# Performance work log

Measured on AMD Instinct MI355X. Metric: run time of the kernel, lower is better.

Reference implementation:

```python
import jax, jax.numpy as jnp
import numpy as np

B = 8
D_IN = 1024
DIM = 256
H = 8
HD = DIM // H
SIZES = [32768, 8192, 2048]
NUM_LEVELS = 3


def setup_inputs() -> dict:
    key = jax.random.key(0)
    ks = jax.random.split(key, 12)
    def p(k, shape, scale=0.02):
        return jax.random.normal(k, shape, dtype=jnp.float32) * scale
    return {
        "x": jax.random.normal(ks[0], (B, D_IN), dtype=jnp.float32),
        "proj_w": p(ks[1], (NUM_LEVELS, DIM, D_IN)),
        "proj_b": p(ks[2], (NUM_LEVELS, DIM)),
        "mem0": p(ks[3], (SIZES[0], DIM), 0.05),
        "mem1": p(ks[4], (SIZES[1], DIM), 0.05),
        "mem2": p(ks[5], (SIZES[2], DIM), 0.05),
        "inw": p(ks[6], (NUM_LEVELS, 3 * DIM, DIM)),
        "inb": p(ks[7], (NUM_LEVELS, 3 * DIM)),
        "outw": p(ks[8], (NUM_LEVELS, DIM, DIM)),
        "outb": p(ks[9], (NUM_LEVELS, DIM)),
        "merg_w": p(ks[10], (D_IN, NUM_LEVELS * DIM)),
        "merg_b": p(ks[11], (D_IN,)),
    }


def _forward(x, proj_w, proj_b, mems, inw, inb, outw, outb, merg_w, merg_b):
    level_outputs = []
    updated_memories = []
    scale = 1.0 / np.sqrt(HD).astype(np.float32)
    for i in range(NUM_LEVELS):
        # per-level projection of x: [B, DIM]
        p = x @ proj_w[i].T + proj_b[i]
        mem = mems[i]  # [S, DIM] (shared across batch, prev_memories=None path)
        wq, wk, wv = inw[i][:DIM], inw[i][DIM:2 * DIM], inw[i][2 * DIM:]
        bq, bk, bv = inb[i][:DIM], inb[i][DIM:2 * DIM], inb[i][2 * DIM:]
        q = (p @ wq.T + bq).reshape(B, H, HD)            # [B, H, HD]
        k = (mem @ wk.T + bk).reshape(-1, H, HD)         # [S, H, HD]
        v = (mem @ wv.T + bv).reshape(-1, H, HD)         # [S, H, HD]
        # single-query attention over the memory bank
        scores = jnp.einsum("bhd,shd->bhs", q, k) * scale   # [B, H, S]
        attn = jax.nn.softmax(scores, axis=-1)
        o = jnp.einsum("bhs,shd->bhd", attn, v).reshape(B, DIM)
        o = o @ outw[i].T + outb[i]                      # attention out_proj
        level_outputs.append(o)
        # broadcast memory update: [B, S, DIM]
        updated_memories.append(mem[None, :, :] + p[:, None, :])
    combined = jnp.concatenate(level_outputs, axis=-1)  # [B, 3*DIM]
    out = combined @ merg_w.T + merg_b                   # [B, D_IN]
    return (out, updated_memories[0], updated_memories[1], updated_memories[2])


def reference(x, proj_w, proj_b, mem0, mem1, mem2, inw, inb, outw, outb, merg_w, merg_b):
    return _forward(x, proj_w, proj_b, (mem0, mem1, mem2), inw, inb, outw, outb, merg_w, merg_b)
```

## Files before the change

### kernel.cpp

```cpp
#include <hip/hip_runtime.h>
#include <math.h>

#define BATCH 8
#define SCALE 0.17677669529663687f

#define WS_P    0
#define WS_QT   6144
#define WS_QBK  55296
#define WS_NUM  55488
#define WS_DEN  104640
#define WS_LVL  104832
#define WS_END  110976
#define WS_ZN   (WS_DEN + 192 - WS_NUM)

#define UM0_F4 2048u
#define UM1_F4 16779264u
#define UM2_F4 20973568u

typedef float f4 __attribute__((ext_vector_type(4)));

__global__ __launch_bounds__(1024) void kA(const float* __restrict__ x,
                                           const float* __restrict__ proj_w,
                                           const float* __restrict__ proj_b,
                                           const float* __restrict__ inw,
                                           const float* __restrict__ inb,
                                           float* __restrict__ ws) {
    const int i = blockIdx.x, b = blockIdx.y, t = threadIdx.x;
    __shared__ __align__(16) float xs[1024];
    __shared__ __align__(16) float ps[256];
    __shared__ __align__(16) float qs[256];
    const int o = t >> 2, part = t & 3;

    {
        const int bid = i * 8 + b;
        const int base = bid * 2056;
        #pragma unroll
        for (int rep = 0; rep < 3; ++rep) {
            const int k = base + rep * 1024 + t;
            if (k < base + 2056 && k < WS_ZN) ws[WS_NUM + k] = 0.f;
        }
    }

    xs[t] = x[b * 1024 + t];
    __syncthreads();

    {
        const f4* w4 = reinterpret_cast<const f4*>(proj_w + (size_t)i * 262144 + (size_t)o * 1024) + part * 64;
        const f4* x4 = reinterpret_cast<const f4*>(xs) + part * 64;
        float acc = 0.f;
        #pragma unroll 8
        for (int c = 0; c < 64; ++c) {
            f4 w = w4[c], xv = x4[c];
            acc += w.x * xv.x + w.y * xv.y + w.z * xv.z + w.w * xv.w;
        }
        acc += __shfl_xor(acc, 1);
        acc += __shfl_xor(acc, 2);
        if (part == 0) {
            const float p = acc + proj_b[i * 256 + o];
            ps[o] = p;
            ws[WS_P + i * 2048 + b * 256 + o] = p;
        }
    }
    __syncthreads();

    {
        const f4* w4 = reinterpret_cast<const f4*>(inw + (size_t)i * 196608 + (size_t)o * 256) + part * 16;
        const f4* p4 = reinterpret_cast<const f4*>(ps) + part * 16;
        float acc = 0.f;
        #pragma unroll
        for (int c = 0; c < 16; ++c) {
            f4 w = w4[c], pv = p4[c];
            acc += w.x * pv.x + w.y * pv.y + w.z * pv.z + w.w * pv.w;
        }
        acc += __shfl_xor(acc, 1);
        acc += __shfl_xor(acc, 2);
        if (part == 0) qs[o] = acc + inb[i * 768 + o];
    }
    __syncthreads();

    #pragma unroll
    for (int rep = 0; rep < 2; ++rep) {
        const int idx = rep * 1024 + t;
        const int h = idx >> 8, c = idx & 255;
        const float* wk = inw + (size_t)i * 196608 + (size_t)(256 + h * 32) * 256 + c;
        float acc = 0.f;
        #pragma unroll
        for (int d = 0; d < 32; ++d) acc += qs[h * 32 + d] * wk[(size_t)d * 256];
        ws[WS_QT + i * 16384 + (b * 8 + h) * 256 + c] = acc * SCALE;
    }
    if (t < 8) {
        float acc = 0.f;
        #pragma unroll
        for (int d = 0; d < 32; ++d) acc += qs[t * 32 + d] * inb[i * 768 + 256 + t * 32 + d];
        ws[WS_QBK + i * 64 + b * 8 + t] = acc * SCALE;
    }
}

__global__ __launch_bounds__(512) void kF(const float* __restrict__ m0,
                                          const float* __restrict__ m1,
                                          const float* __restrict__ m2,
                                          float* __restrict__ ws,
                                          float* __restrict__ out) {
    const int bx = blockIdx.x;
    const int t = threadIdx.x;
    __shared__ __align__(16) f4 lds[2][1024];

    if (bx % 5 == 4) {
        const int aid = bx / 5;
        int lvl, s0;
        const float* mem;
        if (aid < 512)      { lvl = 0; s0 = aid << 6;         mem = m0; }
        else if (aid < 640) { lvl = 1; s0 = (aid - 512) << 6; mem = m1; }
        else                { lvl = 2; s0 = (aid - 640) << 6; mem = m2; }

        const int part = t & 15;
        const int grp = t >> 4;

        f4 qt[2][4];
        const f4* qtb = reinterpret_cast<const f4*>(ws + WS_QT + (size_t)lvl * 16384);
        #pragma unroll
        for (int bl = 0; bl < 2; ++bl)
            #pragma unroll
            for (int g = 0; g < 4; ++g)
                qt[bl][g] = qtb[(size_t)(grp * 2 + bl) * 64 + part + 16 * g];
        float qbk[2];
        #pragma unroll
        for (int bl = 0; bl < 2; ++bl) qbk[bl] = ws[WS_QBK + lvl * 64 + grp * 2 + bl];

        f4 nr[2][4];
        #pragma unroll
        for (int bl = 0; bl < 2; ++bl)
            #pragma unroll
            for (int g = 0; g < 4; ++g) nr[bl][g] = 0.f;
        float dn0 = 0.f, dn1 = 0.f;

        const f4* gm = reinterpret_cast<const f4*>(mem) + (size_t)s0 * 64;
        f4 st[2];
        #pragma unroll
        for (int k = 0; k < 2; ++k) st[k] = gm[t + 512 * k];
        #pragma unroll
        for (int k = 0; k < 2; ++k) lds[0][t + 512 * k] = st[k];
        __syncthreads();

        for (int tile = 0; tile < 4; ++tile) {
            if (tile < 3) {
                #pragma unroll
                for (int k = 0; k < 2; ++k) st[k] = gm[(size_t)(tile + 1) * 1024 + t + 512 * k];
            }
            const f4* buf = lds[tile & 1];
            for (int r = 0; r < 16; ++r) {
                f4 m4[4];
                #pragma unroll
                for (int g = 0; g < 4; ++g) m4[g] = buf[r * 64 + part + 16 * g];
                float sc0 = 0.f, sc1 = 0.f;
                #pragma unroll
                for (int g = 0; g < 4; ++g) {
                    sc0 += qt[0][g].x * m4[g].x + qt[0][g].y * m4[g].y + qt[0][g].z * m4[g].z + qt[0][g].w * m4[g].w;
                    sc1 += qt[1][g].x * m4[g].x + qt[1][g].y * m4[g].y + qt[1][g].z * m4[g].z + qt[1][g].w * m4[g].w;
                }
                sc0 += __shfl_xor(sc0, 1); sc1 += __shfl_xor(sc1, 1);
                sc0 += __shfl_xor(sc0, 2); sc1 += __shfl_xor(sc1, 2);
                sc0 += __shfl_xor(sc0, 4); sc1 += __shfl_xor(sc1, 4);
                sc0 += __shfl_xor(sc0, 8); sc1 += __shfl_xor(sc1, 8);
                const float e0 = __expf(sc0 + qbk[0]);
                const float e1 = __expf(sc1 + qbk[1]);
                dn0 += e0; dn1 += e1;
                #pragma unroll
                for (int g = 0; g < 4; ++g) { nr[0][g] += e0 * m4[g]; nr[1][g] += e1 * m4[g]; }
            }
            if (tile < 3) {
                #pragma unroll
                for (int k = 0; k < 2; ++k) lds[(tile + 1) & 1][t + 512 * k] = st[k];
                __syncthreads();
            }
        }

        #pragma unroll
        for (int bl = 0; bl < 2; ++bl) {
            const int bh = grp * 2 + bl;
            float* np = ws + WS_NUM + (size_t)lvl * 16384 + bh * 256 + part * 4;
            #pragma unroll
            for (int g = 0; g < 4; ++g) {
                #pragma unroll
                for (int j = 0; j < 4; ++j) atomicAdd(np + 64 * g + j, nr[bl][g][j]);
            }
            if (part == 0) atomicAdd(ws + WS_DEN + lvl * 64 + bh, bl == 0 ? dn0 : dn1);
        }
    } else {
        const int wid = (bx / 5) * 4 + (bx % 5);
        int lvl, logS;
        size_t row0, ob4;
        const float* mem;
        if (wid < 2048)      { lvl = 0; row0 = (size_t)wid << 4;          ob4 = UM0_F4; logS = 15; mem = m0; }
        else if (wid < 2560) { lvl = 1; row0 = (size_t)(wid - 2048) << 4; ob4 = UM1_F4; logS = 13; mem = m1; }
        else                 { lvl = 2; row0 = (size_t)(wid - 2560) << 4; ob4 = UM2_F4; logS = 11; mem = m2; }

        const int r = t >> 6;
        const int c4 = t & 63;
        f4 pr[8];
        #pragma unroll
        for (int b = 0; b < 8; ++b)
            pr[b] = reinterpret_cast<const f4*>(ws + WS_P + (size_t)lvl * 2048 + b * 256)[c4];

        const f4* mem4 = reinterpret_cast<const f4*>(mem);
        f4* o4 = reinterpret_cast<f4*>(out) + ob4;

        f4 mv[2];
        #pragma unroll
        for (int k = 0; k < 2; ++k)
            mv[k] = mem4[(row0 + k * 8 + r) * 64 + c4];
        #pragma unroll
        for (int k = 0; k < 2; ++k) {
            const size_t row = row0 + k * 8 + r;
            #pragma unroll
            for (int b = 0; b < 8; ++b)
                o4[((size_t)(b << logS) + row) * 64 + c4] = mv[k] + pr[b];
        }
    }
}

__global__ __launch_bounds__(1024) void kC(const float* __restrict__ inw,
                                           const float* __restrict__ inb,
                                           const float* __restrict__ outw,
                                           const float* __restrict__ outb,
                                           float* __restrict__ ws) {
    const int i = blockIdx.x, b = blockIdx.y, t = threadIdx.x;
    __shared__ __align__(16) float a[2048];
    __shared__ __align__(16) float ao[256];

    #pragma unroll
    for (int rep = 0; rep < 2; ++rep) {
        const int idx = rep * 1024 + t;
        a[idx] = ws[WS_NUM + i * 16384 + b * 2048 + idx] / ws[WS_DEN + i * 64 + b * 8 + (idx >> 8)];
    }
    __syncthreads();

    const int o = t >> 2, part = t & 3;
    {
        const f4* w4 = reinterpret_cast<const f4*>(inw + (size_t)i * 196608 + (size_t)(512 + o) * 256) + part * 16;
        const f4* a4 = reinterpret_cast<const f4*>(a + (o >> 5) * 256) + part * 16;
        float acc = 0.f;
        #pragma unroll
        for (int c = 0; c < 16; ++c) {
            f4 w = w4[c], av = a4[c];
            acc += w.x * av.x + w.y * av.y + w.z * av.z + w.w * av.w;
        }
        acc += __shfl_xor(acc, 1);
        acc += __shfl_xor(acc, 2);
        if (part == 0) ao[o] = acc + inb[i * 768 + 512 + o];
    }
    __syncthreads();
    {
        const f4* w4 = reinterpret_cast<const f4*>(outw + (size_t)i * 65536 + (size_t)o * 256) + part * 16;
        const f4* a4 = reinterpret_cast<const f4*>(ao) + part * 16;
        float acc = 0.f;
        #pragma unroll
        for (int c = 0; c < 16; ++c) {
            f4 w = w4[c], av = a4[c];
            acc += w.x * av.x + w.y * av.y + w.z * av.z + w.w * av.w;
        }
        acc += __shfl_xor(acc, 1);
        acc += __shfl_xor(acc, 2);
        if (part == 0) ws[WS_LVL + i * 2048 + b * 256 + o] = acc + outb[i * 256 + o];
    }
}

__global__ __launch_bounds__(1024) void kD(const float* __restrict__ merg_w,
                                           const float* __restrict__ merg_b,
                                           const float* __restrict__ ws,
                                           float* __restrict__ out) {
    const int b = blockIdx.x, quarter = blockIdx.y, t = threadIdx.x;
    __shared__ __align__(16) float comb[768];
    if (t < 768) comb[t] = ws[WS_LVL + (t >> 8) * 2048 + b * 256 + (t & 255)];
    __syncthreads();

    const int j = quarter * 256 + (t >> 2), part = t & 3;
    const f4* w4 = reinterpret_cast<const f4*>(merg_w + (size_t)j * 768) + part * 48;
    const f4* c4 = reinterpret_cast<const f4*>(comb) + part * 48;
    float acc = 0.f;
    #pragma unroll 8
    for (int c = 0; c < 48; ++c) {
        f4 w = w4[c], cv = c4[c];
        acc += w.x * cv.x + w.y * cv.y + w.z * cv.z + w.w * cv.w;
    }
    acc += __shfl_xor(acc, 1);
    acc += __shfl_xor(acc, 2);
    if (part == 0) out[b * 1024 + j] = acc + merg_b[j];
}

extern "C" void kernel_launch(void* const* d_in, const int* in_sizes, int n_in,
                              void* d_out, int out_size, void* d_ws, size_t ws_size,
                              hipStream_t stream) {
    const float* x      = (const float*)d_in[0];
    const float* proj_w = (const float*)d_in[1];
    const float* proj_b = (const float*)d_in[2];
    const float* mem0   = (const float*)d_in[3];
    const float* mem1   = (const float*)d_in[4];
    const float* mem2   = (const float*)d_in[5];
    const float* inw    = (const float*)d_in[6];
    const float* inb    = (const float*)d_in[7];
    const float* outw   = (const float*)d_in[8];
    const float* outb   = (const float*)d_in[9];
    const float* mw     = (const float*)d_in[10];
    const float* mb     = (const float*)d_in[11];
    float* out = (float*)d_out;
    float* ws  = (float*)d_ws;

    kA<<<dim3(3, 8), 1024, 0, stream>>>(x, proj_w, proj_b, inw, inb, ws);
    kF<<<3360, 512, 0, stream>>>(mem0, mem1, mem2, ws, out);
    kC<<<dim3(3, 8), 1024, 0, stream>>>(inw, inb, outw, outb, ws);
    kD<<<dim3(8, 4), 1024, 0, stream>>>(mw, mb, ws, out);
}
```

Measured before the change: 342.0 us.

## Fuse value/out projection into attention kernel via last-block counter

Removes the separate kC kernel launch. The last attention block to finish, detected by an atomic counter in the workspace, now runs the V-projection and out-projection for all 24 level/batch pairs. The broadcast-update path switches from f4 vector stores to scalar float stores with a different row mapping. The zeroing loop in kA now also clears the counter. This trades one launch gap for a serialized tail on a single 512-thread block doing all 24 projections, and adds a memory-fence dependency.

```diff
diff --git a/kernel.cpp b/kernel.cpp
--- a/kernel.cpp
+++ b/kernel.cpp
@@ -9,13 +9,14 @@
 #define WS_QBK  55296
 #define WS_NUM  55488
 #define WS_DEN  104640
-#define WS_LVL  104832
-#define WS_END  110976
-#define WS_ZN   (WS_DEN + 192 - WS_NUM)
-
-#define UM0_F4 2048u
-#define UM1_F4 16779264u
-#define UM2_F4 20973568u
+#define WS_CNT  104832
+#define WS_LVL  104836
+#define WS_END  110980
+#define WS_ZN   49345
+
+#define UM0_F 8192u
+#define UM1_F 67117056u
+#define UM2_F 83894272u
 
 typedef float f4 __attribute__((ext_vector_type(4)));
 
@@ -33,12 +34,7 @@
 
     {
         const int bid = i * 8 + b;
-        const int base = bid * 2056;
-        #pragma unroll
-        for (int rep = 0; rep < 3; ++rep) {
-            const int k = base + rep * 1024 + t;
-            if (k < base + 2056 && k < WS_ZN) ws[WS_NUM + k] = 0.f;
-        }
+        for (int k = bid * 1024 + t; k < WS_ZN; k += 24576) ws[WS_NUM + k] = 0.f;
     }
 
     xs[t] = x[b * 1024 + t];
@@ -99,11 +95,17 @@
 __global__ __launch_bounds__(512) void kF(const float* __restrict__ m0,
                                           const float* __restrict__ m1,
                                           const float* __restrict__ m2,
+                                          const float* __restrict__ inw,
+                                          const float* __restrict__ inb,
+                                          const float* __restrict__ outw,
+                                          const float* __restrict__ outb,
                                           float* __restrict__ ws,
                                           float* __restrict__ out) {
     const int bx = blockIdx.x;
     const int t = threadIdx.x;
     __shared__ __align__(16) f4 lds[2][1024];
+    __shared__ float dsh[8];
+    __shared__ unsigned int lastflag;
 
     if (bx % 5 == 4) {
         const int aid = bx / 5;
@@ -186,82 +188,84 @@
             }
             if (part == 0) atomicAdd(ws + WS_DEN + lvl * 64 + bh, bl == 0 ? dn0 : dn1);
         }
+
+        __syncthreads();
+        if (t == 0) {
+            __threadfence();
+            unsigned int* cnt = (unsigned int*)(ws + WS_CNT);
+            lastflag = (atomicAdd(cnt, 1u) == 671u) ? 1u : 0u;
+        }
+        __syncthreads();
+        if (lastflag != 1u) return;
+
+        float* af  = reinterpret_cast<float*>(lds);
+        float* aof = af + 2048;
+        const int o = t >> 1, prt = t & 1;
+        for (int ib = 0; ib < 24; ++ib) {
+            const int i = ib >> 3, b = ib & 7;
+            if (t < 8) dsh[t] = atomicAdd(ws + WS_DEN + i * 64 + b * 8 + t, 0.f);
+            float raw[4];
+            #pragma unroll
+            for (int r = 0; r < 4; ++r)
+                raw[r] = atomicAdd(ws + WS_NUM + i * 16384 + b * 2048 + r * 512 + t, 0.f);
+            __syncthreads();
+            #pragma unroll
+            for (int r = 0; r < 4; ++r)
+                af[r * 512 + t] = raw[r] / dsh[(r * 512 + t) >> 8];
+            __syncthreads();
+            {
+                const f4* w4 = reinterpret_cast<const f4*>(inw + (size_t)i * 196608 + (size_t)(512 + o) * 256) + prt * 32;
+                const f4* a4 = reinterpret_cast<const f4*>(af + ((o >> 5) << 8)) + prt * 32;
+                float acc = 0.f;
+                #pragma unroll
+                for (int c = 0; c < 32; ++c) {
+                    f4 w = w4[c], av = a4[c];
+                    acc += w.x * av.x + w.y * av.y + w.z * av.z + w.w * av.w;
+                }
+                acc += __shfl_xor(acc, 1);
+                if (prt == 0) aof[o] = acc + inb[i * 768 + 512 + o];
+            }
+            __syncthreads();
+            {
+                const f4* w4 = reinterpret_cast<const f4*>(outw + (size_t)i * 65536 + (size_t)o * 256) + prt * 32;
+                const f4* a4 = reinterpret_cast<const f4*>(aof) + prt * 32;
+                float acc = 0.f;
+                #pragma unroll
+                for (int c = 0; c < 32; ++c) {
+                    f4 w = w4[c], av = a4[c];
+                    acc += w.x * av.x + w.y * av.y + w.z * av.z + w.w * av.w;
+                }
+                acc += __shfl_xor(acc, 1);
+                if (prt == 0) ws[WS_LVL + i * 2048 + b * 256 + o] = acc + outb[i * 256 + o];
+            }
+            __syncthreads();
+        }
     } else {
         const int wid = (bx / 5) * 4 + (bx % 5);
         int lvl, logS;
-        size_t row0, ob4;
+        size_t row0, obf;
         const float* mem;
-        if (wid < 2048)      { lvl = 0; row0 = (size_t)wid << 4;          ob4 = UM0_F4; logS = 15; mem = m0; }
-        else if (wid < 2560) { lvl = 1; row0 = (size_t)(wid - 2048) << 4; ob4 = UM1_F4; logS = 13; mem = m1; }
-        else                 { lvl = 2; row0 = (size_t)(wid - 2560) << 4; ob4 = UM2_F4; logS = 11; mem = m2; }
-
-        const int r = t >> 6;
-        const int c4 = t & 63;
-        f4 pr[8];
-        #pragma unroll
-        for (int b = 0; b < 8; ++b)
-            pr[b] = reinterpret_cast<const f4*>(ws + WS_P + (size_t)lvl * 2048 + b * 256)[c4];
-
-        const f4* mem4 = reinterpret_cast<const f4*>(mem);
-        f4* o4 = reinterpret_cast<f4*>(out) + ob4;
-
-        f4 mv[2];
-        #pragma unroll
-        for (int k = 0; k < 2; ++k)
-            mv[k] = mem4[(row0 + k * 8 + r) * 64 + c4];
-        #pragma unroll
-        for (int k = 0; k < 2; ++k) {
-            const size_t row = row0 + k * 8 + r;
-            #pragma unroll
-            for (int b = 0; b < 8; ++b)
-                o4[((size_t)(b << logS) + row) * 64 + c4] = mv[k] + pr[b];
-        }
-    }
-}
-
-__global__ __launch_bounds__(1024) void kC(const float* __restrict__ inw,
-                                           const float* __restrict__ inb,
-                                           const float* __restrict__ outw,
-                                           const float* __restrict__ outb,
-                                           float* __restrict__ ws) {
-    const int i = blockIdx.x, b = blockIdx.y, t = threadIdx.x;
-    __shared__ __align__(16) float a[2048];
-    __shared__ __align__(16) float ao[256];
-
-    #pragma unroll
-    for (int rep = 0; rep < 2; ++rep) {
-        const int idx = rep * 1024 + t;
-        a[idx] = ws[WS_NUM + i * 16384 + b * 2048 + idx] / ws[WS_DEN + i * 64 + b * 8 + (idx >> 8)];
-    }
-    __syncthreads();
-
-    const int o = t >> 2, part = t & 3;
-    {
-        const f4* w4 = reinterpret_cast<const f4*>(inw + (size_t)i * 196608 + (size_t)(512 + o) * 256) + part * 16;
-        const f4* a4 = reinterpret_cast<const f4*>(a + (o >> 5) * 256) + part * 16;
-        float acc = 0.f;
-        #pragma unroll
-        for (int c = 0; c < 16; ++c) {
-            f4 w = w4[c], av = a4[c];
-            acc += w.x * av.x + w.y * av.y + w.z * av.z + w.w * av.w;
-        }
-        acc += __shfl_xor(acc, 1);
-        acc += __shfl_xor(acc, 2);
-        if (part == 0) ao[o] = acc + inb[i * 768 + 512 + o];
-    }
-    __syncthreads();
-    {
-        const f4* w4 = reinterpret_cast<const f4*>(outw + (size_t)i * 65536 + (size_t)o * 256) + part * 16;
-        const f4* a4 = reinterpret_cast<const f4*>(ao) + part * 16;
-        float acc = 0.f;
-        #pragma unroll
-        for (int c = 0; c < 16; ++c) {
-            f4 w = w4[c], av = a4[c];
-            acc += w.x * av.x + w.y * av.y + w.z * av.z + w.w * av.w;
-        }
-        acc += __shfl_xor(acc, 1);
-        acc += __shfl_xor(acc, 2);
-        if (part == 0) ws[WS_LVL + i * 2048 + b * 256 + o] = acc + outb[i * 256 + o];
+        if (wid < 2048)      { lvl = 0; row0 = (size_t)wid << 4;          obf = UM0_F; logS = 15; mem = m0; }
+        else if (wid < 2560) { lvl = 1; row0 = (size_t)(wid - 2048) << 4; obf = UM1_F; logS = 13; mem = m1; }
+        else                 { lvl = 2; row0 = (size_t)(wid - 2560) << 4; obf = UM2_F; logS = 11; mem = m2; }
+
+        const int c = t & 255;
+        float pb[8];
+        #pragma unroll
+        for (int b = 0; b < 8; ++b) pb[b] = ws[WS_P + (size_t)lvl * 2048 + b * 256 + c];
+
+        const float* mf = mem + row0 * 256;
+        float* of = out + obf + row0 * 256;
+
+        float v[8];
+        #pragma unroll
+        for (int k = 0; k < 8; ++k) v[k] = mf[k * 512 + t];
+        #pragma unroll
+        for (int b = 0; b < 8; ++b) {
+            float* ob = of + ((size_t)b << (logS + 8));
+            #pragma unroll
+            for (int k = 0; k < 8; ++k) ob[k * 512 + t] = v[k] + pb[b];
+        }
     }
 }
 
@@ -307,7 +311,6 @@
     float* ws  = (float*)d_ws;
 
     kA<<<dim3(3, 8), 1024, 0, stream>>>(x, proj_w, proj_b, inw, inb, ws);
-    kF<<<3360, 512, 0, stream>>>(mem0, mem1, mem2, ws, out);
-    kC<<<dim3(3, 8), 1024, 0, stream>>>(inw, inb, outw, outb, ws);
+    kF<<<3360, 512, 0, stream>>>(mem0, mem1, mem2, inw, inb, outw, outb, ws, out);
     kD<<<dim3(8, 4), 1024, 0, stream>>>(mw, mb, ws, out);
 }
```

Measured after the change: 704.0 us. 2.06x slower.
